# Performance work log

Hardware: AMD Instinct MI355X
Metric: run time of the kernel (lower is better)

## Reference

```python
import jax, jax.numpy as jnp
import numpy as np
from jax import lax

DIM, D_STATE, D_CONV, EXPAND = 96, 16, 4, 2
D_INNER = EXPAND * DIM          # 192
DT_RANK = (DIM + 15) // 16      # 6
B_, T_, H_, W_ = 2, 8, 32, 32   # L = T*H*W = 8192 tokens


def setup_inputs() -> dict:
    key = jax.random.key(0)
    ks = jax.random.split(key, 16)
    f = jnp.float32
    rn = lambda k, shape, s=0.02: jax.random.normal(k, shape, dtype=f) * s
    # S4D-real init for A_log, as in mamba_ssm
    A_init = jnp.log(jnp.tile(jnp.arange(1, D_STATE + 1, dtype=f), (D_INNER, 1)))
    return dict(
        x=jax.random.normal(ks[0], (B_, DIM, T_, H_, W_), dtype=f),
        ln_gamma=1.0 + rn(ks[1], (DIM,)),
        ln_beta=rn(ks[2], (DIM,)),
        in_proj_w=rn(ks[3], (2 * D_INNER, DIM)),
        conv_w=rn(ks[4], (D_INNER, 1, D_CONV), 0.1),
        conv_b=rn(ks[5], (D_INNER,)),
        x_proj_w=rn(ks[6], (DT_RANK + 2 * D_STATE, D_INNER)),
        dt_proj_w=rn(ks[7], (D_INNER, DT_RANK), 0.1),
        dt_proj_b=rn(ks[8], (D_INNER,)) + 0.5,
        A_log=A_init,
        D=jnp.ones((D_INNER,), f),
        conv_w_b=rn(ks[9], (D_INNER, 1, D_CONV), 0.1),
        conv_b_b=rn(ks[10], (D_INNER,)),
        x_proj_w_b=rn(ks[11], (DT_RANK + 2 * D_STATE, D_INNER)),
        dt_proj_w_b=rn(ks[12], (D_INNER, DT_RANK), 0.1),
        dt_proj_b_b=rn(ks[13], (D_INNER,)) + 0.5,
        A_log_b=A_init,
        D_b=jnp.ones((D_INNER,), f),
        out_proj_w=rn(ks[14], (DIM, D_INNER)),
    )


def serpentine(x):
    # continues_scan: reverse W on odd H rows so flattened (T,H,W) ordering is a
    # continuous path through the volume. Involutive => also rev_continues_scan.
    return x.at[..., 1::2, :].set(jnp.flip(x[..., 1::2, :], axis=-1))


def layer_norm(x, g, b, eps=1e-5):
    mu = jnp.mean(x, -1, keepdims=True)
    var = jnp.var(x, -1, keepdims=True)
    return (x - mu) * lax.rsqrt(var + eps) * g + b


def mamba_dir(x_in, z, conv_w, conv_b, x_proj_w, dt_proj_w, dt_proj_b, A_log, D):
    # x_in, z: (B, L, d_inner). One directional selective-scan branch.
    xc = lax.conv_general_dilated(
        x_in.swapaxes(1, 2), conv_w, (1,), [(D_CONV - 1, 0)],
        feature_group_count=D_INNER, dimension_numbers=('NCH', 'OIH', 'NCH'))
    xc = jax.nn.silu(xc + conv_b[None, :, None]).swapaxes(1, 2)  # (B,L,d_inner)
    dbl = jnp.einsum('bld,ed->ble', xc, x_proj_w)                # (B,L,dt_rank+2N)
    dt = jax.nn.softplus(
        jnp.einsum('blr,dr->bld', dbl[..., :DT_RANK], dt_proj_w) + dt_proj_b)
    Bm = dbl[..., DT_RANK:DT_RANK + D_STATE]                     # (B,L,N)
    Cm = dbl[..., DT_RANK + D_STATE:]                            # (B,L,N)
    A = -jnp.exp(A_log)                                          # (d_inner,N)

    def step(h, inp):
        dt_t, x_t, B_t, C_t = inp                                # (B,d),(B,d),(B,N),(B,N)
        h = jnp.exp(dt_t[..., None] * A) * h + (dt_t * x_t)[..., None] * B_t[:, None, :]
        return h, jnp.einsum('bdn,bn->bd', h, C_t)

    h0 = jnp.zeros((x_in.shape[0], D_INNER, D_STATE), x_in.dtype)
    xs = (dt.swapaxes(0, 1), xc.swapaxes(0, 1), Bm.swapaxes(0, 1), Cm.swapaxes(0, 1))
    _, ys = lax.scan(step, h0, xs)                               # (L,B,d_inner)
    y = ys.swapaxes(0, 1) + D * xc
    return y * jax.nn.silu(z)


def reference(x, ln_gamma, ln_beta, in_proj_w, conv_w, conv_b, x_proj_w,
              dt_proj_w, dt_proj_b, A_log, D, conv_w_b, conv_b_b, x_proj_w_b,
              dt_proj_w_b, dt_proj_b_b, A_log_b, D_b, out_proj_w):
    B, C, T, H, W = x.shape
    xs = serpentine(x)
    x_flat = xs.reshape(B, C, T * H * W).swapaxes(1, 2)          # (B,L,dim)
    xn = layer_norm(x_flat, ln_gamma, ln_beta)
    xz = jnp.einsum('bld,ed->ble', xn, in_proj_w)                # (B,L,2*d_inner)
    x_in, z = jnp.split(xz, 2, axis=-1)
    y_f = mamba_dir(x_in, z, conv_w, conv_b, x_proj_w, dt_proj_w,
                    dt_proj_b, A_log, D)
    y_b = jnp.flip(
        mamba_dir(jnp.flip(x_in, 1), jnp.flip(z, 1), conv_w_b, conv_b_b,
                  x_proj_w_b, dt_proj_w_b, dt_proj_b_b, A_log_b, D_b), 1)
    out = jnp.einsum('bld,ed->ble', y_f + y_b, out_proj_w)       # (B,L,dim)
    out = out.swapaxes(1, 2).reshape(B, C, T, H, W)
    return serpentine(out)
```

## Files before the change

### kernel.cpp

```cpp
#include <hip/hip_runtime.h>
#include <math.h>

#define LSEQ 8192
#define TS   32
#define NST  8

template<int CTRL>
__device__ __forceinline__ float dpp_add(float x) {
  const int y = __builtin_amdgcn_update_dpp(0, __float_as_int(x), CTRL, 0xF, 0xF, true);
  return x + __int_as_float(y);
}
__device__ __forceinline__ float red8(float x) {
  x = dpp_add<0xB1>(x);
  x = dpp_add<0x4E>(x);
  x += __int_as_float(__builtin_amdgcn_ds_swizzle(__float_as_int(x), 0x101F));
  return x;
}

__global__ __launch_bounds__(256) void k0_wt(const float* __restrict__ xw_f,
    const float* __restrict__ xw_b, const float* __restrict__ in_w,
    const float* __restrict__ ow, float* __restrict__ xwT,
    float* __restrict__ inwT, float* __restrict__ owT) {
  const int step = gridDim.x * 256;
  const int t0 = blockIdx.x * 256 + threadIdx.x;
  for (int idx = t0; idx < 2 * 192 * 48; idx += step) {
    const int dir = idx / (192 * 48), rem = idx - dir * 192 * 48;
    const int k = rem / 48, r = rem - k * 48;
    const float* w = dir ? xw_b : xw_f;
    xwT[idx] = (r < 38) ? w[r * 192 + k] : 0.f;
  }
  for (int idx = t0; idx < 96 * 384; idx += step) {
    const int k = idx / 384, e = idx - k * 384;
    inwT[idx] = in_w[e * 96 + k];
  }
  for (int idx = t0; idx < 192 * 96; idx += step) {
    const int k = idx / 96, e = idx - k * 96;
    owT[idx] = ow[e * 192 + k];
  }
}

__global__ __launch_bounds__(256) void k1_serp_ln(const float* __restrict__ x,
    const float* __restrict__ gam, const float* __restrict__ bet,
    float* __restrict__ xnT) {
  const int b  = blockIdx.x >> 7;
  const int l0 = (blockIdx.x & 127) << 6;
  __shared__ float xs[96][65];
  __shared__ float mu[64], rs[64];
  const int tid = threadIdx.x;
  for (int idx = tid; idx < 96 * 64; idx += 256) {
    const int c = idx >> 6, l = idx & 63;
    const int lg = l0 + l;
    const int hh = (lg >> 5) & 31, w = lg & 31;
    const int lsrc = (hh & 1) ? (lg + 31 - 2 * w) : lg;
    xs[c][l] = x[(b * 96 + c) * LSEQ + lsrc];
  }
  __syncthreads();
  {
    const int l = tid >> 2, k = tid & 3;
    float s = 0.f, s2 = 0.f;
    for (int c = k; c < 96; c += 4) { const float v = xs[c][l]; s += v; s2 += v * v; }
    s  += __shfl_xor(s, 1);  s  += __shfl_xor(s, 2);
    s2 += __shfl_xor(s2, 1); s2 += __shfl_xor(s2, 2);
    if (k == 0) {
      const float m = s * (1.f / 96.f);
      const float var = s2 * (1.f / 96.f) - m * m;
      mu[l] = m; rs[l] = rsqrtf(var + 1e-5f);
    }
  }
  __syncthreads();
  for (int idx = tid; idx < 96 * 64; idx += 256) {
    const int c = idx >> 6, l = idx & 63;
    xnT[c * 16384 + (b << 13) + l0 + l] =
        (xs[c][l] - mu[l]) * rs[l] * gam[c] + bet[c];
  }
}

__global__ __launch_bounds__(256) void k2_inproj(const float* __restrict__ xnT,
    const float* __restrict__ inwT, float* __restrict__ xz) {
  const int m0 = blockIdx.x << 6;
  const int e0 = blockIdx.y << 6;
  __shared__ float As[96][68];
  __shared__ float Ws[96][68];
  const int tid = threadIdx.x;
  for (int idx = tid; idx < 96 * 64; idx += 256) {
    const int k = idx >> 6, r = idx & 63;
    As[k][r] = xnT[(size_t)k * 16384 + m0 + r];
    Ws[k][r] = inwT[k * 384 + e0 + r];
  }
  __syncthreads();
  const int tx = tid & 15, ty = tid >> 4;
  const int la = tx << 2, ea = ty << 2;
  float acc[4][4] = {};
  for (int k = 0; k < 96; ++k) {
    const float4 av = *(const float4*)&As[k][la];
    const float4 bv = *(const float4*)&Ws[k][ea];
    acc[0][0] = fmaf(bv.x, av.x, acc[0][0]); acc[0][1] = fmaf(bv.x, av.y, acc[0][1]);
    acc[0][2] = fmaf(bv.x, av.z, acc[0][2]); acc[0][3] = fmaf(bv.x, av.w, acc[0][3]);
    acc[1][0] = fmaf(bv.y, av.x, acc[1][0]); acc[1][1] = fmaf(bv.y, av.y, acc[1][1]);
    acc[1][2] = fmaf(bv.y, av.z, acc[1][2]); acc[1][3] = fmaf(bv.y, av.w, acc[1][3]);
    acc[2][0] = fmaf(bv.z, av.x, acc[2][0]); acc[2][1] = fmaf(bv.z, av.y, acc[2][1]);
    acc[2][2] = fmaf(bv.z, av.z, acc[2][2]); acc[2][3] = fmaf(bv.z, av.w, acc[2][3]);
    acc[3][0] = fmaf(bv.w, av.x, acc[3][0]); acc[3][1] = fmaf(bv.w, av.y, acc[3][1]);
    acc[3][2] = fmaf(bv.w, av.z, acc[3][2]); acc[3][3] = fmaf(bv.w, av.w, acc[3][3]);
  }
  const int b = m0 >> 13, l0 = m0 & (LSEQ - 1);
  const bool dos = (e0 >= 192);
#pragma unroll
  for (int j = 0; j < 4; ++j) {
    const int e = e0 + ea + j;
    float4 v;
    v.x = acc[j][0]; v.y = acc[j][1]; v.z = acc[j][2]; v.w = acc[j][3];
    if (dos) {
      v.x = v.x / (1.f + __expf(-v.x)); v.y = v.y / (1.f + __expf(-v.y));
      v.z = v.z / (1.f + __expf(-v.z)); v.w = v.w / (1.f + __expf(-v.w));
    }
    *(float4*)(&xz[((size_t)b * 384 + e) * LSEQ + l0 + la]) = v;
  }
}

__global__ __launch_bounds__(256) void k3a_conv(const float* __restrict__ xz,
    const float* __restrict__ cw_f, const float* __restrict__ cb_f,
    const float* __restrict__ cw_b, const float* __restrict__ cb_b,
    float* __restrict__ xc) {
  const int l = (blockIdx.x << 8) + threadIdx.x;
  const int d = blockIdx.y, b = blockIdx.z;
  const float* xin = xz + ((size_t)b * 384 + d) * LSEQ;
  float xv[7];
#pragma unroll
  for (int j = -3; j <= 3; ++j) {
    const int ls = l + j;
    xv[j + 3] = ((unsigned)ls < LSEQ) ? xin[ls] : 0.f;
  }
  float af = cb_f[d], ab = cb_b[d];
#pragma unroll
  for (int j = 0; j < 4; ++j) {
    af = fmaf(cw_f[d * 4 + j], xv[j], af);
    ab = fmaf(cw_b[d * 4 + j], xv[6 - j], ab);
  }
  xc[((size_t)(b)       * 192 + d) * LSEQ + l] = af / (1.f + __expf(-af));
  xc[((size_t)(2 + b)   * 192 + d) * LSEQ + l] = ab / (1.f + __expf(-ab));
}

__global__ __launch_bounds__(256, 2) void k3b_xproj(const float* __restrict__ xc,
    const float* __restrict__ xwT,
    const float* __restrict__ dtw_f, const float* __restrict__ dtb_f,
    const float* __restrict__ dtw_b, const float* __restrict__ dtb_b,
    float* __restrict__ dt, float* __restrict__ Bo, float* __restrict__ Co) {
  __shared__ float As[48][68];
  __shared__ float Wc[48][48];
  __shared__ float outs[40][68];
  __shared__ float dtwl[1152];
  const int dirb = blockIdx.y, dir = dirb >> 1;
  const int tid = threadIdx.x;
  const int lane = tid & 63, w = tid >> 6;
  const int l0 = blockIdx.x << 6;
  const float* pcBase = xc + (size_t)dirb * 192 * LSEQ + l0;
  const float* wt = xwT + dir * 192 * 48;
  const float* dtwp = dir ? dtw_b : dtw_f;
  for (int idx = tid; idx < 1152; idx += 256) dtwl[idx] = dtwp[idx];
  const int tx = tid & 15, ty = tid >> 4;
  const int la = tx << 2, ra = ty * 3;
  float acc[3][4] = {};
  for (int kc = 0; kc < 192; kc += 48) {
    if (kc) __syncthreads();
    for (int idx = tid; idx < 48 * 64; idx += 256) {
      const int k = idx >> 6, cc = idx & 63;
      As[k][cc] = pcBase[(size_t)(kc + k) * LSEQ + cc];
    }
    for (int idx = tid; idx < 48 * 48; idx += 256) {
      const int k = idx / 48, r = idx - k * 48;
      Wc[k][r] = wt[(kc + k) * 48 + r];
    }
    __syncthreads();
#pragma unroll 4
    for (int k = 0; k < 48; ++k) {
      const float4 a4 = *(const float4*)&As[k][la];
      const float w0 = Wc[k][ra], w1 = Wc[k][ra + 1], w2 = Wc[k][ra + 2];
      acc[0][0] = fmaf(w0, a4.x, acc[0][0]); acc[0][1] = fmaf(w0, a4.y, acc[0][1]);
      acc[0][2] = fmaf(w0, a4.z, acc[0][2]); acc[0][3] = fmaf(w0, a4.w, acc[0][3]);
      acc[1][0] = fmaf(w1, a4.x, acc[1][0]); acc[1][1] = fmaf(w1, a4.y, acc[1][1]);
      acc[1][2] = fmaf(w1, a4.z, acc[1][2]); acc[1][3] = fmaf(w1, a4.w, acc[1][3]);
      acc[2][0] = fmaf(w2, a4.x, acc[2][0]); acc[2][1] = fmaf(w2, a4.y, acc[2][1]);
      acc[2][2] = fmaf(w2, a4.z, acc[2][2]); acc[2][3] = fmaf(w2, a4.w, acc[2][3]);
    }
  }
  __syncthreads();
#pragma unroll
  for (int j = 0; j < 3; ++j) {
    const int r = ra + j;
    if (r < 40) {
#pragma unroll
      for (int i = 0; i < 4; ++i) outs[r][la + i] = acc[j][i];
    }
  }
  __syncthreads();
  {
    const int lq = tid >> 2, g = tid & 3;
    float vB[4], vC[4];
#pragma unroll
    for (int i = 0; i < 4; ++i) {
      vB[i] = outs[6 + 4 * g + i][lq];
      vC[i] = outs[22 + 4 * g + i][lq];
    }
    const size_t off = ((size_t)dirb * LSEQ + l0 + lq) * 16 + 4 * g;
    *(float4*)&Bo[off] = make_float4(vB[0], vB[1], vB[2], vB[3]);
    *(float4*)&Co[off] = make_float4(vC[0], vC[1], vC[2], vC[3]);
  }
  const float* db = dir ? dtb_b : dtb_f;
  const float v0 = outs[0][lane], v1 = outs[1][lane], v2 = outs[2][lane],
              v3 = outs[3][lane], v4 = outs[4][lane], v5 = outs[5][lane];
  float* pdt = dt + (size_t)dirb * 192 * LSEQ + l0 + lane;
#pragma unroll 2
  for (int i = 0; i < 48; ++i) {
    const int d = w * 48 + i;
    float s = db[d];
    s = fmaf(dtwl[d * 6 + 0], v0, s);
    s = fmaf(dtwl[d * 6 + 1], v1, s);
    s = fmaf(dtwl[d * 6 + 2], v2, s);
    s = fmaf(dtwl[d * 6 + 3], v3, s);
    s = fmaf(dtwl[d * 6 + 4], v4, s);
    s = fmaf(dtwl[d * 6 + 5], v5, s);
    pdt[(size_t)d * LSEQ] = (s > 20.f) ? s : __logf(1.f + __expf(s));
  }
}

template<int DIR>
__device__ __forceinline__ void scanA_body(
    float2 (*sdt)[32][34], float (*sb)[TS][16],
    const float* __restrict__ dtg, const float* __restrict__ xcg,
    const float* __restrict__ pB, const float* __restrict__ Al,
    float* __restrict__ Pb, float* __restrict__ Hb, int b, int c, int dg) {
  const int tid = threadIdx.x;
  const int dl = tid >> 3, n = tid & 7;
  const int dirb = DIR * 2 + b;
  const int d = (dg << 5) + dl;
  const float Adn1 = -__expf(Al[d * 16 + n]);
  const float Adn2 = -__expf(Al[d * 16 + n + 8]);
  const size_t rowbase = ((size_t)(dirb * 192) + (dg << 5)) * LSEQ;
  const float* dtp = dtg + rowbase;
  const float* xcp = xcg + rowbase;
  const int c0 = c << 8;
  const int sr0 = tid >> 4, spr = (tid & 15) * 2, sr1 = sr0 + 16;
  const int wt = tid >> 2, wf = (tid & 3) * 4;
  {
    const int tc = c0 + (DIR ? (NST - 1) : 0) * TS;
    const float2 a0 = *(const float2*)&dtp[(size_t)sr0 * LSEQ + tc + spr];
    const float2 x0 = *(const float2*)&xcp[(size_t)sr0 * LSEQ + tc + spr];
    const float2 a1 = *(const float2*)&dtp[(size_t)sr1 * LSEQ + tc + spr];
    const float2 x1 = *(const float2*)&xcp[(size_t)sr1 * LSEQ + tc + spr];
    float4 k0; k0.x = a0.x; k0.y = a0.x * x0.x; k0.z = a0.y; k0.w = a0.y * x0.y;
    float4 k1; k1.x = a1.x; k1.y = a1.x * x1.x; k1.z = a1.y; k1.w = a1.y * x1.y;
    *(float4*)&sdt[0][sr0][spr] = k0;
    *(float4*)&sdt[0][sr1][spr] = k1;
    if (tid < 128) {
      const float4 bv = *(const float4*)&pB[(size_t)(tc + wt) * 16 + wf];
      *(float4*)&sb[0][wt][wf] = bv;
    }
  }
  __syncthreads();
  float h1 = 0.f, h2 = 0.f, dts = 0.f;
  int buf = 0;
  for (int i = 0; i < NST; ++i) {
    const int s = DIR ? (NST - 1 - i) : i;
    float2 a0 = make_float2(0.f, 0.f), x0 = a0, a1 = a0, x1 = a0;
    float4 bv = make_float4(0.f, 0.f, 0.f, 0.f);
    if (i + 1 < NST) {
      const int tn = c0 + (DIR ? (s - 1) : (s + 1)) * TS;
      a0 = *(const float2*)&dtp[(size_t)sr0 * LSEQ + tn + spr];
      x0 = *(const float2*)&xcp[(size_t)sr0 * LSEQ + tn + spr];
      a1 = *(const float2*)&dtp[(size_t)sr1 * LSEQ + tn + spr];
      x1 = *(const float2*)&xcp[(size_t)sr1 * LSEQ + tn + spr];
      if (tid < 128) bv = *(const float4*)&pB[(size_t)(tn + wt) * 16 + wf];
    }
#pragma unroll
    for (int tt = 0; tt < TS; ++tt) {
      const int t = DIR ? (TS - 1 - tt) : tt;
      const float2 xv = sdt[buf][dl][t];
      const float B1 = sb[buf][t][n];
      const float B2 = sb[buf][t][n + 8];
      const float e1 = __expf(xv.x * Adn1);
      const float e2 = __expf(xv.x * Adn2);
      h1 = fmaf(e1, h1, xv.y * B1);
      h2 = fmaf(e2, h2, xv.y * B2);
      dts += xv.x;
    }
    if (i + 1 < NST) {
      float4 k0; k0.x = a0.x; k0.y = a0.x * x0.x; k0.z = a0.y; k0.w = a0.y * x0.y;
      float4 k1; k1.x = a1.x; k1.y = a1.x * x1.x; k1.z = a1.y; k1.w = a1.y * x1.y;
      *(float4*)&sdt[buf ^ 1][sr0][spr] = k0;
      *(float4*)&sdt[buf ^ 1][sr1][spr] = k1;
      if (tid < 128) *(float4*)&sb[buf ^ 1][wt][wf] = bv;
    }
    __syncthreads();
    buf ^= 1;
  }
  const int o = ((dirb * 32 + c) * 192 + d) * 16 + n;
  Pb[o]     = __expf(dts * Adn1);
  Pb[o + 8] = __expf(dts * Adn2);
  Hb[o]     = h1;
  Hb[o + 8] = h2;
}

__global__ __launch_bounds__(256) void k4_scanA(const float* __restrict__ dtg,
    const float* __restrict__ xcg, const float* __restrict__ Bo,
    const float* __restrict__ Al_f, const float* __restrict__ Al_b,
    float* __restrict__ Pb, float* __restrict__ Hb) {
  __shared__ float2 sdt[2][32][34];
  __shared__ float sb[2][TS][16];
  const int b = blockIdx.y, c = blockIdx.x & 31, dg = blockIdx.x >> 5;
  const float* pB0 = Bo + (size_t)(0 * 2 + b) * LSEQ * 16;
  const float* pB1 = Bo + (size_t)(1 * 2 + b) * LSEQ * 16;
  if (blockIdx.z == 0) scanA_body<0>(sdt, sb, dtg, xcg, pB0, Al_f, Pb, Hb, b, c, dg);
  else                 scanA_body<1>(sdt, sb, dtg, xcg, pB1, Al_b, Pb, Hb, b, c, dg);
}

__global__ __launch_bounds__(256) void k5_scanB(const float* __restrict__ Pb,
    const float* __restrict__ Hb, float* __restrict__ H0) {
  const int g = blockIdx.x * 256 + threadIdx.x;
  const int dirb = g / 3072, dn = g - dirb * 3072;
  const int dir = dirb >> 1;
  const int base = dirb * (32 * 3072) + dn;
  float h = 0.f;
  if (dir == 0) {
    for (int c = 0; c < 32; ++c) {
      const int o = base + c * 3072;
      H0[o] = h;
      h = fmaf(Pb[o], h, Hb[o]);
    }
  } else {
    for (int c = 31; c >= 0; --c) {
      const int o = base + c * 3072;
      H0[o] = h;
      h = fmaf(Pb[o], h, Hb[o]);
    }
  }
}

template<int DIR>
__device__ __forceinline__ void scanC_body(
    float2 (*sdt)[32][34], float2 (*sbc)[TS][16],
    const float* __restrict__ dtg, const float* __restrict__ xcg,
    const float* __restrict__ pB, const float* __restrict__ pC,
    const float* __restrict__ xz,
    const float* __restrict__ Al, const float* __restrict__ Dv_,
    const float* __restrict__ H0, float* __restrict__ yout,
    int b, int c, int dg) {
  const int tid = threadIdx.x;
  const int dl = tid >> 3, n = tid & 7;
  const int dirb = DIR * 2 + b;
  const int d = (dg << 5) + dl;
  const float Adn1 = -__expf(Al[d * 16 + n]);
  const float Adn2 = -__expf(Al[d * 16 + n + 8]);
  const float Dv = Dv_[d];
  const size_t rowbase = ((size_t)(dirb * 192) + (dg << 5)) * LSEQ;
  const float* dtp = dtg + rowbase;
  const float* xcp = xcg + rowbase;
  const float* xcq = xcg + ((size_t)(dirb * 192) + d) * LSEQ;
  const float* psp = xz + ((size_t)(b * 384) + 192 + d) * LSEQ;
  float* py = yout + ((size_t)(b * 192) + d) * LSEQ;
  const int o = ((dirb * 32 + c) * 192 + d) * 16 + n;
  float h1 = H0[o], h2 = H0[o + 8];
  const int c0 = c << 8;
  const int sr0 = tid >> 4, spr = (tid & 15) * 2, sr1 = sr0 + 16;
  const int sbt = tid >> 3, sbp = (tid & 7) * 2;
  float cx0, cx1, cx2, cx3, sp0, sp1, sp2, sp3;
  {
    const int tc = c0 + (DIR ? (NST - 1) : 0) * TS;
    const float2 a0 = *(const float2*)&dtp[(size_t)sr0 * LSEQ + tc + spr];
    const float2 x0 = *(const float2*)&xcp[(size_t)sr0 * LSEQ + tc + spr];
    const float2 a1 = *(const float2*)&dtp[(size_t)sr1 * LSEQ + tc + spr];
    const float2 x1 = *(const float2*)&xcp[(size_t)sr1 * LSEQ + tc + spr];
    const float2 b2 = *(const float2*)&pB[(size_t)(tc + sbt) * 16 + sbp];
    const float2 c2 = *(const float2*)&pC[(size_t)(tc + sbt) * 16 + sbp];
    float4 k0; k0.x = a0.x; k0.y = a0.x * x0.x; k0.z = a0.y; k0.w = a0.y * x0.y;
    float4 k1; k1.x = a1.x; k1.y = a1.x * x1.x; k1.z = a1.y; k1.w = a1.y * x1.y;
    *(float4*)&sdt[0][sr0][spr] = k0;
    *(float4*)&sdt[0][sr1][spr] = k1;
    *(float4*)&sbc[0][sbt][sbp] = make_float4(b2.x, c2.x, b2.y, c2.y);
    cx0 = xcq[tc + n];      cx1 = xcq[tc + 8 + n];
    cx2 = xcq[tc + 16 + n]; cx3 = xcq[tc + 24 + n];
    sp0 = psp[tc + n];      sp1 = psp[tc + 8 + n];
    sp2 = psp[tc + 16 + n]; sp3 = psp[tc + 24 + n];
  }
  __syncthreads();
  int buf = 0;
  for (int i = 0; i < NST; ++i) {
    const int s = DIR ? (NST - 1 - i) : i;
    const int t0 = c0 + s * TS;
    float2 a0 = make_float2(0.f, 0.f), x0 = a0, a1 = a0, x1 = a0, b2 = a0, c2 = a0;
    float nx0 = 0.f, nx1 = 0.f, nx2 = 0.f, nx3 = 0.f;
    float ns0 = 0.f, ns1 = 0.f, ns2 = 0.f, ns3 = 0.f;
    if (i + 1 < NST) {
      const int tn = c0 + (DIR ? (s - 1) : (s + 1)) * TS;
      a0 = *(const float2*)&dtp[(size_t)sr0 * LSEQ + tn + spr];
      x0 = *(const float2*)&xcp[(size_t)sr0 * LSEQ + tn + spr];
      a1 = *(const float2*)&dtp[(size_t)sr1 * LSEQ + tn + spr];
      x1 = *(const float2*)&xcp[(size_t)sr1 * LSEQ + tn + spr];
      b2 = *(const float2*)&pB[(size_t)(tn + sbt) * 16 + sbp];
      c2 = *(const float2*)&pC[(size_t)(tn + sbt) * 16 + sbp];
      nx0 = xcq[tn + n];      nx1 = xcq[tn + 8 + n];
      nx2 = xcq[tn + 16 + n]; nx3 = xcq[tn + 24 + n];
      ns0 = psp[tn + n];      ns1 = psp[tn + 8 + n];
      ns2 = psp[tn + 16 + n]; ns3 = psp[tn + 24 + n];
    }
    float pq0 = 0.f, pq1 = 0.f, pq2 = 0.f, pq3 = 0.f;
#pragma unroll
    for (int tt = 0; tt < TS; ++tt) {
      const int t = DIR ? (TS - 1 - tt) : tt;
      const float2 xv = sdt[buf][dl][t];
      const float2 v1 = sbc[buf][t][n];
      const float2 v2 = sbc[buf][t][n + 8];
      const float e1 = __expf(xv.x * Adn1);
      const float e2 = __expf(xv.x * Adn2);
      h1 = fmaf(e1, h1, xv.y * v1.x);
      h2 = fmaf(e2, h2, xv.y * v2.x);
      float p = fmaf(h2, v2.y, h1 * v1.y);
      p = red8(p);
      const bool m = ((t & 7) == n);
      if ((t >> 3) == 0)      pq0 = m ? p : pq0;
      else if ((t >> 3) == 1) pq1 = m ? p : pq1;
      else if ((t >> 3) == 2) pq2 = m ? p : pq2;
      else                    pq3 = m ? p : pq3;
    }
    py[t0 + n]      = fmaf(Dv, cx0, pq0) * sp0;
    py[t0 + 8 + n]  = fmaf(Dv, cx1, pq1) * sp1;
    py[t0 + 16 + n] = fmaf(Dv, cx2, pq2) * sp2;
    py[t0 + 24 + n] = fmaf(Dv, cx3, pq3) * sp3;
    if (i + 1 < NST) {
      float4 k0; k0.x = a0.x; k0.y = a0.x * x0.x; k0.z = a0.y; k0.w = a0.y * x0.y;
      float4 k1; k1.x = a1.x; k1.y = a1.x * x1.x; k1.z = a1.y; k1.w = a1.y * x1.y;
      *(float4*)&sdt[buf ^ 1][sr0][spr] = k0;
      *(float4*)&sdt[buf ^ 1][sr1][spr] = k1;
      *(float4*)&sbc[buf ^ 1][sbt][sbp] = make_float4(b2.x, c2.x, b2.y, c2.y);
      cx0 = nx0; cx1 = nx1; cx2 = nx2; cx3 = nx3;
      sp0 = ns0; sp1 = ns1; sp2 = ns2; sp3 = ns3;
    }
    __syncthreads();
    buf ^= 1;
  }
}

__global__ __launch_bounds__(256) void k6_scanC(const float* __restrict__ dtg,
    const float* __restrict__ xcg, const float* __restrict__ Bo,
    const float* __restrict__ Co, const float* __restrict__ xz,
    const float* __restrict__ Al_f, const float* __restrict__ Al_b,
    const float* __restrict__ D_f, const float* __restrict__ D_b,
    const float* __restrict__ H0,
    float* __restrict__ yf, float* __restrict__ yb) {
  __shared__ float2 sdt[2][32][34];
  __shared__ float2 sbc[2][TS][16];
  const int b = blockIdx.y, c = blockIdx.x & 31, dg = blockIdx.x >> 5;
  const float* pB0 = Bo + (size_t)(0 * 2 + b) * LSEQ * 16;
  const float* pB1 = Bo + (size_t)(1 * 2 + b) * LSEQ * 16;
  const float* pC0 = Co + (size_t)(0 * 2 + b) * LSEQ * 16;
  const float* pC1 = Co + (size_t)(1 * 2 + b) * LSEQ * 16;
  if (blockIdx.z == 0)
    scanC_body<0>(sdt, sbc, dtg, xcg, pB0, pC0, xz, Al_f, D_f, H0, yf, b, c, dg);
  else
    scanC_body<1>(sdt, sbc, dtg, xcg, pB1, pC1, xz, Al_b, D_b, H0, yb, b, c, dg);
}

__global__ __launch_bounds__(256) void k7_outproj(const float* __restrict__ yf,
    const float* __restrict__ yb, const float* __restrict__ owT,
    float* __restrict__ out) {
  const int m0 = blockIdx.x << 6;
  const int e0 = blockIdx.y * 48;
  const int b = m0 >> 13, l0 = m0 & (LSEQ - 1);
  __shared__ float As[48][68];
  __shared__ float Ws[48][49];
  const int tid = threadIdx.x;
  const int tx = tid & 15, ty = tid >> 4;
  const int la = tx << 2, ea = ty * 3;
  float acc[3][4] = {};
  for (int kc = 0; kc < 192; kc += 48) {
    for (int idx = tid; idx < 48 * 64; idx += 256) {
      const int k = idx >> 6, l = idx & 63;
      const size_t off = ((size_t)b * 192 + kc + k) * LSEQ + l0 + l;
      As[k][l] = yf[off] + yb[off];
    }
    for (int idx = tid; idx < 48 * 48; idx += 256) {
      const int k = idx / 48, e = idx - k * 48;
      Ws[k][e] = owT[(kc + k) * 96 + e0 + e];
    }
    __syncthreads();
#pragma unroll 4
    for (int k = 0; k < 48; ++k) {
      const float4 a4 = *(const float4*)&As[k][la];
      const float w0 = Ws[k][ea], w1 = Ws[k][ea + 1], w2 = Ws[k][ea + 2];
      acc[0][0] = fmaf(w0, a4.x, acc[0][0]); acc[0][1] = fmaf(w0, a4.y, acc[0][1]);
      acc[0][2] = fmaf(w0, a4.z, acc[0][2]); acc[0][3] = fmaf(w0, a4.w, acc[0][3]);
      acc[1][0] = fmaf(w1, a4.x, acc[1][0]); acc[1][1] = fmaf(w1, a4.y, acc[1][1]);
      acc[1][2] = fmaf(w1, a4.z, acc[1][2]); acc[1][3] = fmaf(w1, a4.w, acc[1][3]);
      acc[2][0] = fmaf(w2, a4.x, acc[2][0]); acc[2][1] = fmaf(w2, a4.y, acc[2][1]);
      acc[2][2] = fmaf(w2, a4.z, acc[2][2]); acc[2][3] = fmaf(w2, a4.w, acc[2][3]);
    }
    __syncthreads();
  }
#pragma unroll
  for (int j = 0; j < 3; ++j) {
    const int e = e0 + ea + j;
#pragma unroll
    for (int i = 0; i < 4; ++i) {
      const int l = l0 + la + i;
      const int hh = (l >> 5) & 31, ww = l & 31;
      const int lp = (hh & 1) ? (l + 31 - 2 * ww) : l;
      out[((size_t)b * 96 + e) * LSEQ + lp] = acc[j][i];
    }
  }
}

extern "C" void kernel_launch(void* const* d_in, const int* in_sizes, int n_in,
                              void* d_out, int out_size, void* d_ws, size_t ws_size,
                              hipStream_t stream) {
  const float* x     = (const float*)d_in[0];
  const float* ln_g  = (const float*)d_in[1];
  const float* ln_b  = (const float*)d_in[2];
  const float* in_w  = (const float*)d_in[3];
  const float* cw_f  = (const float*)d_in[4];
  const float* cb_f  = (const float*)d_in[5];
  const float* xw_f  = (const float*)d_in[6];
  const float* dtw_f = (const float*)d_in[7];
  const float* dtb_f = (const float*)d_in[8];
  const float* Al_f  = (const float*)d_in[9];
  const float* D_f   = (const float*)d_in[10];
  const float* cw_b  = (const float*)d_in[11];
  const float* cb_b  = (const float*)d_in[12];
  const float* xw_b  = (const float*)d_in[13];
  const float* dtw_b = (const float*)d_in[14];
  const float* dtb_b = (const float*)d_in[15];
  const float* Al_b  = (const float*)d_in[16];
  const float* D_b   = (const float*)d_in[17];
  const float* ow    = (const float*)d_in[18];
  float* out = (float*)d_out;

  float* ws = (float*)d_ws;
  float* xnT  = ws; ws += (size_t)16384 * 96;
  float* xz   = ws; ws += (size_t)2 * 384 * LSEQ;
  float* xc   = ws; ws += (size_t)4 * 192 * LSEQ;
  float* dt   = ws; ws += (size_t)4 * 192 * LSEQ;
  float* Bo   = ws; ws += (size_t)4 * LSEQ * 16;
  float* Co   = ws; ws += (size_t)4 * LSEQ * 16;
  float* yf   = ws; ws += (size_t)2 * 192 * LSEQ;
  float* yb   = ws; ws += (size_t)2 * 192 * LSEQ;
  float* Pb   = ws; ws += (size_t)4 * 32 * 192 * 16;
  float* Hb   = ws; ws += (size_t)4 * 32 * 192 * 16;
  float* H0   = ws; ws += (size_t)4 * 32 * 192 * 16;
  float* xwT  = ws; ws += (size_t)2 * 192 * 48;
  float* inwT = ws; ws += (size_t)96 * 384;
  float* owT  = ws; ws += (size_t)192 * 96;

  k0_wt<<<dim3(64), dim3(256), 0, stream>>>(xw_f, xw_b, in_w, ow, xwT, inwT, owT);
  k1_serp_ln<<<dim3(256), dim3(256), 0, stream>>>(x, ln_g, ln_b, xnT);
  k2_inproj<<<dim3(256, 6), dim3(256), 0, stream>>>(xnT, inwT, xz);
  k3a_conv<<<dim3(32, 192, 2), dim3(256), 0, stream>>>(xz, cw_f, cb_f, cw_b, cb_b, xc);
  k3b_xproj<<<dim3(128, 4), dim3(256), 0, stream>>>(xc, xwT,
      dtw_f, dtb_f, dtw_b, dtb_b, dt, Bo, Co);
  k4_scanA<<<dim3(192, 2, 2), dim3(256), 0, stream>>>(dt, xc, Bo,
      Al_f, Al_b, Pb, Hb);
  k5_scanB<<<dim3(48), dim3(256), 0, stream>>>(Pb, Hb, H0);
  k6_scanC<<<dim3(192, 2, 2), dim3(256), 0, stream>>>(dt, xc, Bo, Co,
      xz, Al_f, Al_b, D_f, D_b, H0, yf, yb);
  k7_outproj<<<dim3(256, 2), dim3(256), 0, stream>>>(yf, yb, owT, out);
}
```

Before: 189.8 us.

## Split x_proj into separate GEMM and dt/B/C expansion kernels

```diff
diff --git a/kernel.cpp b/kernel.cpp
--- a/kernel.cpp
+++ b/kernel.cpp
@@ -23,9 +23,9 @@
     float* __restrict__ inwT, float* __restrict__ owT) {
   const int step = gridDim.x * 256;
   const int t0 = blockIdx.x * 256 + threadIdx.x;
-  for (int idx = t0; idx < 2 * 192 * 48; idx += step) {
-    const int dir = idx / (192 * 48), rem = idx - dir * 192 * 48;
-    const int k = rem / 48, r = rem - k * 48;
+  for (int idx = t0; idx < 2 * 192 * 64; idx += step) {
+    const int dir = idx / (192 * 64), rem = idx - dir * 192 * 64;
+    const int k = rem >> 6, r = rem & 63;
     const float* w = dir ? xw_b : xw_f;
     xwT[idx] = (r < 38) ? w[r * 192 + k] : 0.f;
   }
@@ -141,76 +141,81 @@
   xc[((size_t)(2 + b)   * 192 + d) * LSEQ + l] = ab / (1.f + __expf(-ab));
 }
 
-__global__ __launch_bounds__(256, 2) void k3b_xproj(const float* __restrict__ xc,
-    const float* __restrict__ xwT,
+__global__ __launch_bounds__(256) void k3b1_xproj(const float* __restrict__ xc,
+    const float* __restrict__ xwT, float* __restrict__ dbl) {
+  const int dirb = blockIdx.x >> 7, dir = dirb >> 1;
+  const int l0 = (blockIdx.x & 127) << 6;
+  __shared__ float As[96][68];
+  __shared__ float Ws[96][68];
+  const int tid = threadIdx.x;
+  const float* pcBase = xc + (size_t)dirb * 192 * LSEQ + l0;
+  const float* wt = xwT + dir * 192 * 64;
+  const int tx = tid & 15, ty = tid >> 4;
+  const int la = tx << 2, ea = ty << 2;
+  float acc[4][4] = {};
+  for (int kc = 0; kc < 192; kc += 96) {
+    if (kc) __syncthreads();
+    for (int idx = tid; idx < 96 * 64; idx += 256) {
+      const int k = idx >> 6, r = idx & 63;
+      As[k][r] = pcBase[(size_t)(kc + k) * LSEQ + r];
+      Ws[k][r] = wt[(kc + k) * 64 + r];
+    }
+    __syncthreads();
+    for (int k = 0; k < 96; ++k) {
+      const float4 av = *(const float4*)&As[k][la];
+      const float4 bv = *(const float4*)&Ws[k][ea];
+      acc[0][0] = fmaf(bv.x, av.x, acc[0][0]); acc[0][1] = fmaf(bv.x, av.y, acc[0][1]);
+      acc[0][2] = fmaf(bv.x, av.z, acc[0][2]); acc[0][3] = fmaf(bv.x, av.w, acc[0][3]);
+      acc[1][0] = fmaf(bv.y, av.x, acc[1][0]); acc[1][1] = fmaf(bv.y, av.y, acc[1][1]);
+      acc[1][2] = fmaf(bv.y, av.z, acc[1][2]); acc[1][3] = fmaf(bv.y, av.w, acc[1][3]);
+      acc[2][0] = fmaf(bv.z, av.x, acc[2][0]); acc[2][1] = fmaf(bv.z, av.y, acc[2][1]);
+      acc[2][2] = fmaf(bv.z, av.z, acc[2][2]); acc[2][3] = fmaf(bv.z, av.w, acc[2][3]);
+      acc[3][0] = fmaf(bv.w, av.x, acc[3][0]); acc[3][1] = fmaf(bv.w, av.y, acc[3][1]);
+      acc[3][2] = fmaf(bv.w, av.z, acc[3][2]); acc[3][3] = fmaf(bv.w, av.w, acc[3][3]);
+    }
+  }
+#pragma unroll
+  for (int j = 0; j < 4; ++j) {
+    const int r = ea + j;
+    if (r < 40) {
+      float4 v;
+      v.x = acc[j][0]; v.y = acc[j][1]; v.z = acc[j][2]; v.w = acc[j][3];
+      *(float4*)(&dbl[((size_t)dirb * 40 + r) * LSEQ + l0 + la]) = v;
+    }
+  }
+}
+
+__global__ __launch_bounds__(256) void k3b2_dtbc(const float* __restrict__ dbl,
     const float* __restrict__ dtw_f, const float* __restrict__ dtb_f,
     const float* __restrict__ dtw_b, const float* __restrict__ dtb_b,
     float* __restrict__ dt, float* __restrict__ Bo, float* __restrict__ Co) {
-  __shared__ float As[48][68];
-  __shared__ float Wc[48][48];
-  __shared__ float outs[40][68];
   __shared__ float dtwl[1152];
   const int dirb = blockIdx.y, dir = dirb >> 1;
   const int tid = threadIdx.x;
   const int lane = tid & 63, w = tid >> 6;
   const int l0 = blockIdx.x << 6;
-  const float* pcBase = xc + (size_t)dirb * 192 * LSEQ + l0;
-  const float* wt = xwT + dir * 192 * 48;
   const float* dtwp = dir ? dtw_b : dtw_f;
   for (int idx = tid; idx < 1152; idx += 256) dtwl[idx] = dtwp[idx];
-  const int tx = tid & 15, ty = tid >> 4;
-  const int la = tx << 2, ra = ty * 3;
-  float acc[3][4] = {};
-  for (int kc = 0; kc < 192; kc += 48) {
-    if (kc) __syncthreads();
-    for (int idx = tid; idx < 48 * 64; idx += 256) {
-      const int k = idx >> 6, cc = idx & 63;
-      As[k][cc] = pcBase[(size_t)(kc + k) * LSEQ + cc];
-    }
-    for (int idx = tid; idx < 48 * 48; idx += 256) {
-      const int k = idx / 48, r = idx - k * 48;
-      Wc[k][r] = wt[(kc + k) * 48 + r];
-    }
-    __syncthreads();
-#pragma unroll 4
-    for (int k = 0; k < 48; ++k) {
-      const float4 a4 = *(const float4*)&As[k][la];
-      const float w0 = Wc[k][ra], w1 = Wc[k][ra + 1], w2 = Wc[k][ra + 2];
-      acc[0][0] = fmaf(w0, a4.x, acc[0][0]); acc[0][1] = fmaf(w0, a4.y, acc[0][1]);
-      acc[0][2] = fmaf(w0, a4.z, acc[0][2]); acc[0][3] = fmaf(w0, a4.w, acc[0][3]);
-      acc[1][0] = fmaf(w1, a4.x, acc[1][0]); acc[1][1] = fmaf(w1, a4.y, acc[1][1]);
-      acc[1][2] = fmaf(w1, a4.z, acc[1][2]); acc[1][3] = fmaf(w1, a4.w, acc[1][3]);
-      acc[2][0] = fmaf(w2, a4.x, acc[2][0]); acc[2][1] = fmaf(w2, a4.y, acc[2][1]);
-      acc[2][2] = fmaf(w2, a4.z, acc[2][2]); acc[2][3] = fmaf(w2, a4.w, acc[2][3]);
-    }
-  }
-  __syncthreads();
-#pragma unroll
-  for (int j = 0; j < 3; ++j) {
-    const int r = ra + j;
-    if (r < 40) {
-#pragma unroll
-      for (int i = 0; i < 4; ++i) outs[r][la + i] = acc[j][i];
-    }
-  }
-  __syncthreads();
+  const float* pd = dbl + (size_t)dirb * 40 * LSEQ + l0;
   {
     const int lq = tid >> 2, g = tid & 3;
     float vB[4], vC[4];
 #pragma unroll
     for (int i = 0; i < 4; ++i) {
-      vB[i] = outs[6 + 4 * g + i][lq];
-      vC[i] = outs[22 + 4 * g + i][lq];
+      vB[i] = pd[(size_t)(6 + 4 * g + i) * LSEQ + lq];
+      vC[i] = pd[(size_t)(22 + 4 * g + i) * LSEQ + lq];
     }
     const size_t off = ((size_t)dirb * LSEQ + l0 + lq) * 16 + 4 * g;
     *(float4*)&Bo[off] = make_float4(vB[0], vB[1], vB[2], vB[3]);
     *(float4*)&Co[off] = make_float4(vC[0], vC[1], vC[2], vC[3]);
   }
+  const float v0 = pd[(size_t)0 * LSEQ + lane], v1 = pd[(size_t)1 * LSEQ + lane],
+              v2 = pd[(size_t)2 * LSEQ + lane], v3 = pd[(size_t)3 * LSEQ + lane],
+              v4 = pd[(size_t)4 * LSEQ + lane], v5 = pd[(size_t)5 * LSEQ + lane];
+  __syncthreads();
   const float* db = dir ? dtb_b : dtb_f;
-  const float v0 = outs[0][lane], v1 = outs[1][lane], v2 = outs[2][lane],
-              v3 = outs[3][lane], v4 = outs[4][lane], v5 = outs[5][lane];
   float* pdt = dt + (size_t)dirb * 192 * LSEQ + l0 + lane;
-#pragma unroll 2
+#pragma unroll 4
   for (int i = 0; i < 48; ++i) {
     const int d = w * 48 + i;
     float s = db[d];
@@ -538,6 +543,7 @@
   float* xz   = ws; ws += (size_t)2 * 384 * LSEQ;
   float* xc   = ws; ws += (size_t)4 * 192 * LSEQ;
   float* dt   = ws; ws += (size_t)4 * 192 * LSEQ;
+  float* dbl  = ws; ws += (size_t)4 * 40 * LSEQ;
   float* Bo   = ws; ws += (size_t)4 * LSEQ * 16;
   float* Co   = ws; ws += (size_t)4 * LSEQ * 16;
   float* yf   = ws; ws += (size_t)2 * 192 * LSEQ;
@@ -545,7 +551,7 @@
   float* Pb   = ws; ws += (size_t)4 * 32 * 192 * 16;
   float* Hb   = ws; ws += (size_t)4 * 32 * 192 * 16;
   float* H0   = ws; ws += (size_t)4 * 32 * 192 * 16;
-  float* xwT  = ws; ws += (size_t)2 * 192 * 48;
+  float* xwT  = ws; ws += (size_t)2 * 192 * 64;
   float* inwT = ws; ws += (size_t)96 * 384;
   float* owT  = ws; ws += (size_t)192 * 96;
 
@@ -553,7 +559,8 @@
   k1_serp_ln<<<dim3(256), dim3(256), 0, stream>>>(x, ln_g, ln_b, xnT);
   k2_inproj<<<dim3(256, 6), dim3(256), 0, stream>>>(xnT, inwT, xz);
   k3a_conv<<<dim3(32, 192, 2), dim3(256), 0, stream>>>(xz, cw_f, cb_f, cw_b, cb_b, xc);
-  k3b_xproj<<<dim3(128, 4), dim3(256), 0, stream>>>(xc, xwT,
+  k3b1_xproj<<<dim3(512), dim3(256), 0, stream>>>(xc, xwT, dbl);
+  k3b2_dtbc<<<dim3(128, 4), dim3(256), 0, stream>>>(dbl,
       dtw_f, dtb_f, dtw_b, dtb_b, dt, Bo, Co);
   k4_scanA<<<dim3(192, 2, 2), dim3(256), 0, stream>>>(dt, xc, Bo,
       Al_f, Al_b, Pb, Hb);
```

New measurement: 178.4 us. -6.0%, faster.
